# Kernel optimization log

Measured on AMD Instinct MI355X. Metric: run time of the kernel, lower is better.

The kernel has to match this reference:

```python
import jax, jax.numpy as jnp
import numpy as np

EMBED_DIM = 768
NUM_HEADS = 12
HEAD_DIM = EMBED_DIM // NUM_HEADS
SCALING = HEAD_DIM ** (-0.5)


def setup_inputs() -> dict:
    key = jax.random.key(0)
    ks = jax.random.split(key, 10)
    R, C, B, E = 128, 256, 1, EMBED_DIM
    x = jax.random.normal(ks[0], (R, C, B, E), dtype=jnp.float32)
    pad_mask = jax.random.randint(ks[1], (B, C), 0, 2).astype(bool)
    s = 1.0 / np.sqrt(E)
    wq = jax.random.normal(ks[2], (E, E), dtype=jnp.float32) * s
    bq = jnp.zeros((E,), dtype=jnp.float32)
    wk = jax.random.normal(ks[3], (E, E), dtype=jnp.float32) * s
    bk = jnp.zeros((E,), dtype=jnp.float32)
    wv = jax.random.normal(ks[4], (E, E), dtype=jnp.float32) * s
    bv = jnp.zeros((E,), dtype=jnp.float32)
    wo = jax.random.normal(ks[5], (E, E), dtype=jnp.float32) * s
    bo = jnp.zeros((E,), dtype=jnp.float32)
    return {"x": x, "self_attn_padding_mask": pad_mask,
            "wq": wq, "bq": bq, "wk": wk, "bk": bk,
            "wv": wv, "bv": bv, "wo": wo, "bo": bo}


def reference(x, self_attn_padding_mask, wq, bq, wk, bk, wv, bv, wo, bo):
    # x: [num_rows R, num_cols C, batch B, embed E]
    R, C, B, E = x.shape
    H, D = NUM_HEADS, HEAD_DIM
    q = (x @ wq.T + bq).reshape(R, C, B, H, D) * SCALING
    k = (x @ wk.T + bk).reshape(R, C, B, H, D)
    v = (x @ wv.T + bv).reshape(R, C, B, H, D)
    # attention over rows, independent per column c and batch n
    attn_weights = jnp.einsum('icnhd,jcnhd->hcnij', q, k)  # [H,C,B,R,R]
    if self_attn_padding_mask is not None:
        # mask: [B,C] -> mask all keys j for padded columns (same for all j)
        m = self_attn_padding_mask.T[None, :, :, None, None]  # [1,C,B,1,1]
        attn_weights = jnp.where(m, jnp.float32(-10000.0), attn_weights)
    attn_probs = jax.nn.softmax(attn_weights, axis=-1)
    context = jnp.einsum('hcnij,jcnhd->icnhd', attn_probs, v)
    context = context.reshape(R, C, B, E)
    output = context @ wo.T + bo
    return output, attn_probs
```

## Files before the change

### kernel.cpp

```cpp
#include <hip/hip_runtime.h>


typedef __attribute__((ext_vector_type(8))) __bf16 bf16x8;
typedef __attribute__((ext_vector_type(4))) float f32x4;
typedef unsigned short u16;
typedef unsigned int u32;

constexpr size_t TE = (size_t)32768 * 768;
constexpr int VSTRIDE = 256 * 1536;

__device__ __forceinline__ u16 f2b(float f) {
    u32 u = __builtin_bit_cast(u32, f);
    u += 0x7FFFu + ((u >> 16) & 1u);
    return (u16)(u >> 16);
}
__device__ __forceinline__ void split2(float f, u16& h, u16& l) {
    u32 u = __builtin_bit_cast(u32, f);
    h = (u16)(u >> 16);
    float rest = f - __builtin_bit_cast(float, u & 0xFFFF0000u);
    l = (u16)(__builtin_bit_cast(u32, rest) >> 16);
}

union B8 { bf16x8 v; u16 s[8]; uint4 q; };

__global__ __launch_bounds__(256) void convert_w3(
    const float* __restrict__ Wq, const float* __restrict__ Wk,
    const float* __restrict__ Wv, u16* __restrict__ slots)
{
    const int m = blockIdx.y;
    const float* src = (m == 0) ? Wq : ((m == 1) ? Wk : Wv);
    const int idx = blockIdx.x * 256 + threadIdx.x;
    const int r = idx / 96, k0 = (idx % 96) * 8;
    float4 f0 = *(const float4*)(src + (size_t)r * 768 + k0);
    float4 f1 = *(const float4*)(src + (size_t)r * 768 + k0 + 4);
    B8 h, l;
    split2(f0.x, h.s[0], l.s[0]); split2(f0.y, h.s[1], l.s[1]);
    split2(f0.z, h.s[2], l.s[2]); split2(f0.w, h.s[3], l.s[3]);
    split2(f1.x, h.s[4], l.s[4]); split2(f1.y, h.s[5], l.s[5]);
    split2(f1.z, h.s[6], l.s[6]); split2(f1.w, h.s[7], l.s[7]);
    *(uint4*)&slots[(size_t)1536 * (m * 1536 + r) + k0] = h.q;
    *(uint4*)&slots[(size_t)1536 * (m * 1536 + 768 + r) + k0] = l.q;
}

template <int MODE>
__global__ __launch_bounds__(256) void gemm_proj(
    const float* __restrict__ A, const u16* __restrict__ wsl, int wbase,
    const float* __restrict__ bias, u16* __restrict__ dst, float scale)
{
    const int tn = blockIdx.x;
    const int tm = blockIdx.y;
    const int tid = threadIdx.x;
    const int lane = tid & 63, w = tid >> 6;
    const int l16 = lane & 15, quad = lane >> 4;
    const int wr = w >> 1, wc = w & 1;

    __shared__ u16 Ah[4][128][8], Al[4][128][8];

    f32x4 acc[4][4];
#pragma unroll
    for (int a = 0; a < 4; ++a)
#pragma unroll
        for (int b = 0; b < 4; ++b) acc[a][b] = (f32x4){0.f, 0.f, 0.f, 0.f};

    for (int k0 = 0; k0 < 768; k0 += 32) {
#pragma unroll
        for (int it = 0; it < 4; ++it) {
            int v = tid + 256 * it;
            int row = v >> 3, kq = v & 7;
            float4 a4 = *(const float4*)(A + ((size_t)tm * 128 + row) * 768 + k0 + kq * 4);
            int c8 = kq >> 1, o4 = (kq & 1) * 4;
            u16 h0,h1,h2,h3,l0,l1,l2,l3;
            split2(a4.x,h0,l0); split2(a4.y,h1,l1); split2(a4.z,h2,l2); split2(a4.w,h3,l3);
            *(uint2*)&Ah[c8][row][o4] = make_uint2((u32)h0|((u32)h1<<16),(u32)h2|((u32)h3<<16));
            *(uint2*)&Al[c8][row][o4] = make_uint2((u32)l0|((u32)l1<<16),(u32)l2|((u32)l3<<16));
        }
        __syncthreads();
        bf16x8 ah[4], al[4], bh[4], bl[4];
#pragma unroll
        for (int a = 0; a < 4; ++a) {
            ah[a] = *(const bf16x8*)&Ah[quad][64 * wr + 16 * a + l16][0];
            al[a] = *(const bf16x8*)&Al[quad][64 * wr + 16 * a + l16][0];
        }
#pragma unroll
        for (int b = 0; b < 4; ++b) {
            int n = tn * 128 + 64 * wc + 16 * b + l16;
            bh[b] = *(const bf16x8*)&wsl[(size_t)1536 * (wbase + n) + k0 + quad * 8];
            bl[b] = *(const bf16x8*)&wsl[(size_t)1536 * (wbase + 768 + n) + k0 + quad * 8];
        }
#pragma unroll
        for (int a = 0; a < 4; ++a)
#pragma unroll
            for (int b = 0; b < 4; ++b) {
                acc[a][b] = __builtin_amdgcn_mfma_f32_16x16x32_bf16(ah[a], bh[b], acc[a][b], 0, 0, 0);
                acc[a][b] = __builtin_amdgcn_mfma_f32_16x16x32_bf16(ah[a], bl[b], acc[a][b], 0, 0, 0);
                acc[a][b] = __builtin_amdgcn_mfma_f32_16x16x32_bf16(al[a], bh[b], acc[a][b], 0, 0, 0);
            }
        __syncthreads();
    }

#pragma unroll
    for (int b = 0; b < 4; ++b) {
        int n = tn * 128 + 64 * wc + 16 * b + l16;
        float bs = bias[n];
#pragma unroll
        for (int a = 0; a < 4; ++a) {
#pragma unroll
            for (int r = 0; r < 4; ++r) {
                int row = 64 * wr + 16 * a + quad * 4 + r;
                int t = tm * 128 + row;
                float val = (acc[a][b][r] + bs) * scale;
                if (MODE == 2) {
                    dst[(size_t)t * 1536 + 768 + n] = f2b(val);
                } else {
                    int i = t >> 8, cc = t & 255;
                    int hh = n >> 6, d = n & 63;
                    u16* win = dst + (((size_t)hh * 256 + cc) << 15);
                    int base = (MODE == 0 ? 0 : 16384);
                    u16 vh, vl; split2(val, vh, vl);
                    win[base + i * 64 + d] = vh;
                    win[base + 8192 + i * 64 + d] = vl;
                }
            }
        }
    }
}

__global__ __launch_bounds__(256) void attn_kernel(
    u16* __restrict__ winU,
    u16* __restrict__ slots,
    const int* __restrict__ maskg)
{
    const int blk = blockIdx.x;
    const int c = blk & 255, h = blk >> 8;
    const int tid = threadIdx.x;
    const int lane = tid & 63, w = tid >> 6;
    const int l16 = lane & 15, quad = lane >> 4;

    __shared__ u16 kbuf[2][8][128][8];
    __shared__ u16 vsT[16][64][8];
    u16 (*ps)[128][8] = (u16(*)[128][8])&kbuf[0][0][0][0];

    u16* win = winU + (((size_t)h * 256 + c) << 15);
    float* winF = (float*)win;

#pragma unroll
    for (int it = 0; it < 4; ++it) {
        int v = tid + 256 * it;
        int j = v >> 3, d0 = (v & 7) * 8;
        *(uint4*)&kbuf[0][d0 >> 3][j][0] = *(const uint4*)(win + 16384 + j * 64 + d0);
        *(uint4*)&kbuf[1][d0 >> 3][j][0] = *(const uint4*)(win + 24576 + j * 64 + d0);
    }
    const u16* vb = slots + (size_t)c * 1536 + 768 + h * 64;
#pragma unroll
    for (int it = 0; it < 4; ++it) {
        int v = tid + 256 * it;
        int j = v >> 3, d0 = (v & 7) * 8;
        B8 t; t.q = *(const uint4*)(vb + (size_t)j * VSTRIDE + d0);
#pragma unroll
        for (int e = 0; e < 8; ++e) vsT[j >> 3][d0 + e][j & 7] = t.s[e];
    }
    __syncthreads();

    f32x4 s[2][8];
#pragma unroll
    for (int a = 0; a < 2; ++a)
#pragma unroll
        for (int jb = 0; jb < 8; ++jb) s[a][jb] = (f32x4){0.f, 0.f, 0.f, 0.f};

#pragma unroll
    for (int kc = 0; kc < 2; ++kc) {
        bf16x8 qh[2], ql[2];
#pragma unroll
        for (int a = 0; a < 2; ++a) {
            int i = 32 * w + 16 * a + l16;
            qh[a] = *(const bf16x8*)(win + i * 64 + kc * 32 + quad * 8);
            ql[a] = *(const bf16x8*)(win + 8192 + i * 64 + kc * 32 + quad * 8);
        }
#pragma unroll
        for (int jb = 0; jb < 8; ++jb) {
            bf16x8 kh = *(const bf16x8*)&kbuf[0][kc * 4 + quad][16 * jb + l16][0];
            bf16x8 kl = *(const bf16x8*)&kbuf[1][kc * 4 + quad][16 * jb + l16][0];
#pragma unroll
            for (int a = 0; a < 2; ++a) {
                s[a][jb] = __builtin_amdgcn_mfma_f32_16x16x32_bf16(qh[a], kh, s[a][jb], 0, 0, 0);
                s[a][jb] = __builtin_amdgcn_mfma_f32_16x16x32_bf16(qh[a], kl, s[a][jb], 0, 0, 0);
                s[a][jb] = __builtin_amdgcn_mfma_f32_16x16x32_bf16(ql[a], kh, s[a][jb], 0, 0, 0);
            }
        }
    }

    if (maskg[c] != 0) {
#pragma unroll
        for (int a = 0; a < 2; ++a)
#pragma unroll
            for (int jb = 0; jb < 8; ++jb) s[a][jb] = (f32x4){0.f, 0.f, 0.f, 0.f};
    }

#pragma unroll
    for (int a = 0; a < 2; ++a) {
#pragma unroll
        for (int r = 0; r < 4; ++r) {
            float m = s[a][0][r];
#pragma unroll
            for (int jb = 1; jb < 8; ++jb) m = fmaxf(m, s[a][jb][r]);
#pragma unroll
            for (int off = 1; off < 16; off <<= 1) m = fmaxf(m, __shfl_xor(m, off, 64));
            float sum = 0.f;
#pragma unroll
            for (int jb = 0; jb < 8; ++jb) {
                float e = expf(s[a][jb][r] - m);
                s[a][jb][r] = e;
                sum += e;
            }
#pragma unroll
            for (int off = 1; off < 16; off <<= 1) sum += __shfl_xor(sum, off, 64);
            float inv = 1.f / sum;
#pragma unroll
            for (int jb = 0; jb < 8; ++jb) s[a][jb][r] *= inv;
        }
    }

    __syncthreads();

#pragma unroll
    for (int a = 0; a < 2; ++a)
#pragma unroll
        for (int jb = 0; jb < 8; ++jb)
#pragma unroll
            for (int r = 0; r < 4; ++r) {
                int i = 32 * w + 16 * a + quad * 4 + r;
                int j = 16 * jb + l16;
                float pv = s[a][jb][r];
                winF[i * 128 + j] = pv;
                ps[j >> 3][i][j & 7] = f2b(pv);
            }
    __syncthreads();

    f32x4 o[2][4];
#pragma unroll
    for (int a = 0; a < 2; ++a)
#pragma unroll
        for (int b = 0; b < 4; ++b) o[a][b] = (f32x4){0.f, 0.f, 0.f, 0.f};

#pragma unroll
    for (int kc = 0; kc < 4; ++kc) {
        bf16x8 ap[2];
#pragma unroll
        for (int a = 0; a < 2; ++a)
            ap[a] = *(const bf16x8*)&ps[kc * 4 + quad][32 * w + 16 * a + l16][0];
#pragma unroll
        for (int b = 0; b < 4; ++b) {
            bf16x8 bv = *(const bf16x8*)&vsT[kc * 4 + quad][16 * b + l16][0];
#pragma unroll
            for (int a = 0; a < 2; ++a)
                o[a][b] = __builtin_amdgcn_mfma_f32_16x16x32_bf16(ap[a], bv, o[a][b], 0, 0, 0);
        }
    }

#pragma unroll
    for (int a = 0; a < 2; ++a)
#pragma unroll
        for (int b = 0; b < 4; ++b)
#pragma unroll
            for (int r = 0; r < 4; ++r) {
                int i = 32 * w + 16 * a + quad * 4 + r;
                int d = 16 * b + l16;
                slots[(size_t)(i * 256 + c) * 1536 + h * 64 + d] = f2b(o[a][b][r]);
            }
}

__global__ __launch_bounds__(256) void gemm_out(
    const u16* __restrict__ slots, const float* __restrict__ W,
    const float* __restrict__ bias, float* __restrict__ out0, int nb)
{
    const int t0 = blockIdx.x * 64;
    const int tid = threadIdx.x;
    const int lane = tid & 63, w = tid >> 6;
    const int l16 = lane & 15, quad = lane >> 4;

    __shared__ u16 cs[2][4][64][8];

    f32x4 acc[4][6];
#pragma unroll
    for (int a = 0; a < 4; ++a)
#pragma unroll
        for (int jt = 0; jt < 6; ++jt) acc[a][jt] = (f32x4){0.f, 0.f, 0.f, 0.f};

    const int srow = tid >> 2, sk8 = tid & 3;
    const u16* sp = slots + (size_t)(t0 + srow) * 1536 + sk8 * 8;

    *(uint4*)&cs[0][sk8][srow][0] = *(const uint4*)(sp);
    for (int kc = 0; kc < 24; ++kc) {
        const int buf = kc & 1;
        __syncthreads();
        if (kc + 1 < 24)
            *(uint4*)&cs[buf ^ 1][sk8][srow][0] = *(const uint4*)(sp + (kc + 1) * 32);

        bf16x8 af[4];
#pragma unroll
        for (int a = 0; a < 4; ++a)
            af[a] = *(const bf16x8*)&cs[buf][quad][16 * a + l16][0];

#pragma unroll
        for (int jt = 0; jt < 6; ++jt) {
            int n = nb + 96 * w + 16 * jt + l16;
            const float* wp = W + (size_t)n * 768 + kc * 32 + quad * 8;
            float4 f0 = *(const float4*)(wp);
            float4 f1 = *(const float4*)(wp + 4);
            B8 wh, wl;
            split2(f0.x, wh.s[0], wl.s[0]); split2(f0.y, wh.s[1], wl.s[1]);
            split2(f0.z, wh.s[2], wl.s[2]); split2(f0.w, wh.s[3], wl.s[3]);
            split2(f1.x, wh.s[4], wl.s[4]); split2(f1.y, wh.s[5], wl.s[5]);
            split2(f1.z, wh.s[6], wl.s[6]); split2(f1.w, wh.s[7], wl.s[7]);
#pragma unroll
            for (int a = 0; a < 4; ++a) {
                acc[a][jt] = __builtin_amdgcn_mfma_f32_16x16x32_bf16(af[a], wh.v, acc[a][jt], 0, 0, 0);
                acc[a][jt] = __builtin_amdgcn_mfma_f32_16x16x32_bf16(af[a], wl.v, acc[a][jt], 0, 0, 0);
            }
        }
    }

#pragma unroll
    for (int jt = 0; jt < 6; ++jt) {
        int n = nb + 96 * w + 16 * jt + l16;
        float bs = bias[n];
#pragma unroll
        for (int a = 0; a < 4; ++a) {
#pragma unroll
            for (int r = 0; r < 4; ++r) {
                int row = 16 * a + quad * 4 + r;
                out0[(size_t)(t0 + row) * 768 + n] = acc[a][jt][r] + bs;
            }
        }
    }
}

extern "C" void kernel_launch(void* const* d_in, const int* in_sizes, int n_in,
                              void* d_out, int out_size, void* d_ws, size_t ws_size,
                              hipStream_t stream) {
    const float* x    = (const float*)d_in[0];
    const int*   mask = (const int*)d_in[1];
    const float* wq = (const float*)d_in[2];
    const float* bq = (const float*)d_in[3];
    const float* wk = (const float*)d_in[4];
    const float* bk = (const float*)d_in[5];
    const float* wv = (const float*)d_in[6];
    const float* bv = (const float*)d_in[7];
    const float* wo = (const float*)d_in[8];
    const float* bo = (const float*)d_in[9];

    float* out0  = (float*)d_out;
    u16*   slots = (u16*)d_out;
    u16*   winU  = (u16*)(out0 + TE);

    dim3 blk(256);
    convert_w3<<<dim3(288, 3), blk, 0, stream>>>(wq, wk, wv, slots);
    dim3 grid(6, 256);
    gemm_proj<0><<<grid, blk, 0, stream>>>(x, slots, 0,    bq, winU,  0.125f);
    gemm_proj<1><<<grid, blk, 0, stream>>>(x, slots, 1536, bk, winU,  1.0f);
    gemm_proj<2><<<grid, blk, 0, stream>>>(x, slots, 3072, bv, slots, 1.0f);
    attn_kernel<<<dim3(12 * 256), blk, 0, stream>>>(winU, slots, mask);
    gemm_out<<<dim3(512), blk, 0, stream>>>(slots, wo, bo, out0, 384);
    gemm_out<<<dim3(512), blk, 0, stream>>>(slots, wo, bo, out0, 0);
}
```

Before: 1.356 ms.

## Double-buffer A tiles with register prefetch, swizzle LDS, remap blocks per XCD

The projection GEMM now stages A tiles through two LDS buffers. The next k-chunk's fp32 loads are issued into registers before the MFMAs and split/stored after them, so global latency overlaps compute and one barrier per iteration is dropped. The LDS layout is XOR-swizzled to cut bank conflicts on the bf16x8 reads. The grid is flattened to 1D and remapped so consecutive tiles of an XCD share A rows, which should improve L2 reuse. The cost is higher register pressure from the prefetch buffers and twice the LDS footprint.

```diff
diff --git a/kernel.cpp b/kernel.cpp
--- a/kernel.cpp
+++ b/kernel.cpp
@@ -47,14 +47,14 @@
     const float* __restrict__ A, const u16* __restrict__ wsl, int wbase,
     const float* __restrict__ bias, u16* __restrict__ dst, float scale)
 {
-    const int tn = blockIdx.x;
-    const int tm = blockIdx.y;
+    const int wg = ((blockIdx.x & 7) * 192) + (blockIdx.x >> 3);
+    const int tm = wg / 6, tn = wg - tm * 6;
     const int tid = threadIdx.x;
     const int lane = tid & 63, w = tid >> 6;
     const int l16 = lane & 15, quad = lane >> 4;
     const int wr = w >> 1, wc = w & 1;
 
-    __shared__ u16 Ah[4][128][8], Al[4][128][8];
+    __shared__ u16 Ah[2][128][4][8], Al[2][128][4][8];
 
     f32x4 acc[4][4];
 #pragma unroll
@@ -62,31 +62,57 @@
 #pragma unroll
         for (int b = 0; b < 4; ++b) acc[a][b] = (f32x4){0.f, 0.f, 0.f, 0.f};
 
-    for (int k0 = 0; k0 < 768; k0 += 32) {
-#pragma unroll
-        for (int it = 0; it < 4; ++it) {
-            int v = tid + 256 * it;
-            int row = v >> 3, kq = v & 7;
-            float4 a4 = *(const float4*)(A + ((size_t)tm * 128 + row) * 768 + k0 + kq * 4);
-            int c8 = kq >> 1, o4 = (kq & 1) * 4;
-            u16 h0,h1,h2,h3,l0,l1,l2,l3;
-            split2(a4.x,h0,l0); split2(a4.y,h1,l1); split2(a4.z,h2,l2); split2(a4.w,h3,l3);
-            *(uint2*)&Ah[c8][row][o4] = make_uint2((u32)h0|((u32)h1<<16),(u32)h2|((u32)h3<<16));
-            *(uint2*)&Al[c8][row][o4] = make_uint2((u32)l0|((u32)l1<<16),(u32)l2|((u32)l3<<16));
-        }
-        __syncthreads();
-        bf16x8 ah[4], al[4], bh[4], bl[4];
-#pragma unroll
-        for (int a = 0; a < 4; ++a) {
-            ah[a] = *(const bf16x8*)&Ah[quad][64 * wr + 16 * a + l16][0];
-            al[a] = *(const bf16x8*)&Al[quad][64 * wr + 16 * a + l16][0];
-        }
+    const int row0 = tid >> 3, kq = tid & 7;
+    const int c8 = kq >> 1, o4 = (kq & 1) * 4;
+    const float* ap = A + ((size_t)tm * 128 + row0) * 768 + kq * 4;
+
+    float4 pf[4];
+#define LOADA(k0) do {                                                        \
+    _Pragma("unroll")                                                         \
+    for (int it = 0; it < 4; ++it)                                            \
+        pf[it] = *(const float4*)(ap + (k0) + (size_t)it * 32 * 768);         \
+} while (0)
+
+#define STAGE(buf) do {                                                       \
+    _Pragma("unroll")                                                         \
+    for (int it = 0; it < 4; ++it) {                                          \
+        int row = row0 + 32 * it;                                             \
+        int sw = c8 ^ (((row >> 1) ^ (row >> 3)) & 3);                        \
+        u16 h0,h1,h2,h3,l0,l1,l2,l3;                                          \
+        split2(pf[it].x,h0,l0); split2(pf[it].y,h1,l1);                       \
+        split2(pf[it].z,h2,l2); split2(pf[it].w,h3,l3);                       \
+        *(uint2*)&Ah[buf][row][sw][o4] =                                      \
+            make_uint2((u32)h0|((u32)h1<<16),(u32)h2|((u32)h3<<16));          \
+        *(uint2*)&Al[buf][row][sw][o4] =                                      \
+            make_uint2((u32)l0|((u32)l1<<16),(u32)l2|((u32)l3<<16));          \
+    }                                                                         \
+} while (0)
+
+    LOADA(0);
+    STAGE(0);
+    __syncthreads();
+
+    for (int kc = 0; kc < 24; ++kc) {
+        const int buf = kc & 1;
+        const int k0 = kc * 32;
+
+        bf16x8 bh[4], bl[4];
 #pragma unroll
         for (int b = 0; b < 4; ++b) {
             int n = tn * 128 + 64 * wc + 16 * b + l16;
             bh[b] = *(const bf16x8*)&wsl[(size_t)1536 * (wbase + n) + k0 + quad * 8];
             bl[b] = *(const bf16x8*)&wsl[(size_t)1536 * (wbase + 768 + n) + k0 + quad * 8];
         }
+        if (kc < 23) LOADA(k0 + 32);
+
+        bf16x8 ah[4], al[4];
+#pragma unroll
+        for (int a = 0; a < 4; ++a) {
+            int row = 64 * wr + 16 * a + l16;
+            int sw = quad ^ (((row >> 1) ^ (row >> 3)) & 3);
+            ah[a] = *(const bf16x8*)&Ah[buf][row][sw][0];
+            al[a] = *(const bf16x8*)&Al[buf][row][sw][0];
+        }
 #pragma unroll
         for (int a = 0; a < 4; ++a)
 #pragma unroll
@@ -95,8 +121,11 @@
                 acc[a][b] = __builtin_amdgcn_mfma_f32_16x16x32_bf16(ah[a], bl[b], acc[a][b], 0, 0, 0);
                 acc[a][b] = __builtin_amdgcn_mfma_f32_16x16x32_bf16(al[a], bh[b], acc[a][b], 0, 0, 0);
             }
+        if (kc < 23) STAGE(buf ^ 1);
         __syncthreads();
     }
+#undef LOADA
+#undef STAGE
 
 #pragma unroll
     for (int b = 0; b < 4; ++b) {
@@ -355,10 +384,9 @@
 
     dim3 blk(256);
     convert_w3<<<dim3(288, 3), blk, 0, stream>>>(wq, wk, wv, slots);
-    dim3 grid(6, 256);
-    gemm_proj<0><<<grid, blk, 0, stream>>>(x, slots, 0,    bq, winU,  0.125f);
-    gemm_proj<1><<<grid, blk, 0, stream>>>(x, slots, 1536, bk, winU,  1.0f);
-    gemm_proj<2><<<grid, blk, 0, stream>>>(x, slots, 3072, bv, slots, 1.0f);
+    gemm_proj<0><<<dim3(1536), blk, 0, stream>>>(x, slots, 0,    bq, winU,  0.125f);
+    gemm_proj<1><<<dim3(1536), blk, 0, stream>>>(x, slots, 1536, bk, winU,  1.0f);
+    gemm_proj<2><<<dim3(1536), blk, 0, stream>>>(x, slots, 3072, bv, slots, 1.0f);
     attn_kernel<<<dim3(12 * 256), blk, 0, stream>>>(winU, slots, mask);
     gemm_out<<<dim3(512), blk, 0, stream>>>(slots, wo, bo, out0, 384);
     gemm_out<<<dim3(512), blk, 0, stream>>>(slots, wo, bo, out0, 0);
```

New measurement: 1.338 ms. About the same (-1.3%).
